# Kernel tuning notes

Hardware: AMD Instinct MI355X
Metric: run time of the kernel (lower is better)

Reference implementation:

```python
import math
import jax, jax.numpy as jnp
import numpy as np

# config (matches env defaults of the torch module, scaled to production size)
V, D, L, NH, NKV, MLP_M, RECUR, N_VB = 32768, 1024, 6, 16, 8, 3, 2, 5
BG_BK, BG_DIM = 4096, 128
HD = D // NH            # 64 head dim
KV = NKV * HD           # 512 kv width
B, T = 2, 1024
SOFTCAP = 30.0
EPS = 1.1920929e-07     # fp32 eps used by F.rms_norm(eps=None)


def _rms(x):
    return x * jax.lax.rsqrt(jnp.mean(jnp.square(x), axis=-1, keepdims=True) + EPS)


def _rope(x, c, s):
    h = x.shape[-1] // 2
    x1, x2 = x[..., :h], x[..., h:]
    return jnp.concatenate([x1 * c + x2 * s, -x1 * s + x2 * c], axis=-1)


def _forward(ids, tgt, emb, bg_embed, bg_proj, bg_scale, ve,
             Wq, Wk, Wv, Wo, qg, a_s, m_s, mix, Wfc, Wpr):
    Bz, Tz = ids.shape
    # token embedding + bigram-hash embedding
    x = emb[ids]
    t = ids.astype(jnp.int32)
    hv = jnp.bitwise_xor(t[:, 1:] * 36313, t[:, :-1] * 27191) % (BG_BK - 1)
    h = jnp.zeros_like(t).at[:, 1:].set(hv)
    bg = (bg_embed[h] @ bg_proj) * bg_scale
    x = _rms(x + bg)
    x0 = x
    # rope tables
    inv = 1.0 / (10000.0 ** (jnp.arange(0, HD, 2, dtype=jnp.float32) / HD))
    ang = jnp.arange(Tz, dtype=jnp.float32)[:, None] * inv      # (T, HD/2)
    c, s = jnp.cos(ang)[None, None], jnp.sin(ang)[None, None]   # (1,1,T,HD/2)
    mask = jnp.tril(jnp.ones((Tz, Tz), dtype=bool))
    eff = 0
    for _ in range(RECUR):
        for l in range(L):
            vel = ve[eff % N_VB][ids]                            # (B,T,KV)
            m = mix[l]
            x = m[0] * x + m[1] * x0
            # attention
            xn = _rms(x)
            q = (xn @ Wq[l]).reshape(Bz, Tz, NH, HD).transpose(0, 2, 1, 3)
            k = (xn @ Wk[l]).reshape(Bz, Tz, NKV, HD).transpose(0, 2, 1, 3)
            v = ((xn @ Wv[l]) + vel).reshape(Bz, Tz, NKV, HD).transpose(0, 2, 1, 3)
            q, k = _rms(q), _rms(k)
            q, k = _rope(q, c, s), _rope(k, c, s)
            q = q * qg[l][None, :, None, None]
            rep = NH // NKV                                      # GQA expand
            kf = jnp.repeat(k, rep, axis=1)
            vf = jnp.repeat(v, rep, axis=1)
            sc = jnp.einsum('bhqd,bhkd->bhqk', q, kf) / math.sqrt(HD)
            sc = jnp.where(mask, sc, -jnp.inf)
            att = jax.nn.softmax(sc, axis=-1)
            y = jnp.einsum('bhqk,bhkd->bhqd', att, vf)
            y = y.transpose(0, 2, 1, 3).reshape(Bz, Tz, D) @ Wo[l]
            x = x + a_s[l] * y
            # mlp: relu(fc(x))^2 @ proj
            hmid = jnp.square(jax.nn.relu(_rms(x) @ Wfc[l]))
            x = x + m_s[l] * (hmid @ Wpr[l])
            eff += 1
    x = _rms(x)
    lo = x @ emb.T
    lo = SOFTCAP * jnp.tanh(lo / SOFTCAP)
    logp = jax.nn.log_softmax(lo, axis=-1)
    nll = -jnp.take_along_axis(logp, tgt[..., None], axis=-1)[..., 0]
    return jnp.mean(nll)


def setup_inputs() -> dict:
    key = jax.random.key(0)
    ks = jax.random.split(key, 14)
    def nrm(k, shape, std):
        return std * jax.random.normal(k, shape, dtype=jnp.float32)
    eff = L * RECUR
    return {
        'ids': jax.random.randint(ks[0], (B, T), 0, V),
        'tgt': jax.random.randint(ks[1], (B, T), 0, V),
        'emb': nrm(ks[2], (V, D), 0.005),
        'bg_embed': nrm(ks[3], (BG_BK, BG_DIM), 0.02),
        'bg_proj': nrm(ks[4], (BG_DIM, D), 1.0 / math.sqrt(BG_DIM)),
        'bg_scale': jnp.float32(0.05),
        've': nrm(ks[5], (N_VB, V, KV), 0.01),
        'Wq': nrm(ks[6], (L, D, D), 1.0 / math.sqrt(D)),
        'Wk': nrm(ks[7], (L, D, KV), 1.0 / math.sqrt(D)),
        'Wv': nrm(ks[8], (L, D, KV), 1.0 / math.sqrt(D)),
        'Wo': nrm(ks[9], (L, D, D), 1.0 / (math.sqrt(D) * math.sqrt(2 * eff))),
        'qg': jnp.full((L, NH), 1.5, jnp.float32),
        'a_s': jnp.ones((L, D), jnp.float32),
        'm_s': jnp.ones((L, D), jnp.float32),
        'mix': jnp.stack([jnp.ones((L, D)), jnp.zeros((L, D))], axis=1).astype(jnp.float32),
        'Wfc': nrm(ks[10], (L, D, MLP_M * D), 1.0 / math.sqrt(D)),
        'Wpr': nrm(ks[11], (L, MLP_M * D, D), 1.0 / (math.sqrt(MLP_M * D) * math.sqrt(2 * eff))),
    }


def reference(ids, tgt, emb, bg_embed, bg_proj, bg_scale, ve,
              Wq, Wk, Wv, Wo, qg, a_s, m_s, mix, Wfc, Wpr):
    return _forward(ids, tgt, emb, bg_embed, bg_proj, bg_scale, ve,
                    Wq, Wk, Wv, Wo, qg, a_s, m_s, mix, Wfc, Wpr)
```

## Files before the change

kernel.cpp:

```cpp
#include <hip/hip_runtime.h>
#include <hip/hip_bf16.h>
#include <math.h>

#define DEV __device__ __forceinline__

typedef unsigned short u16;
typedef short bf16x8 __attribute__((ext_vector_type(8)));
typedef float f32x4 __attribute__((ext_vector_type(4)));
typedef u16 u16x8 __attribute__((ext_vector_type(8)));
typedef u16 u16x4 __attribute__((ext_vector_type(4)));

#define T_SEQ 1024
#define NTOK 2048
#define DIM 1024
#define NHD 16
#define NKVH 8
#define HDIM 64
#define KVD 512
#define MLPD 3072
#define VOC 32768
#define EPSF 1.1920929e-07f
#define SCAP 30.0f
#define NCB 512
#define PSTRIDE ((size_t)NTOK * DIM)

#define MEMFENCE asm volatile("" ::: "memory")

DEV u16 f2b(float f) {
  __hip_bfloat16 h = __float2bfloat16(f);
  u16 r; __builtin_memcpy(&r, &h, 2); return r;
}
DEV float b2f(u16 u) {
  __hip_bfloat16 h; __builtin_memcpy(&h, &u, 2);
  return __bfloat162float(h);
}

DEV void gload16(const void* g, void* l) {
  __builtin_amdgcn_global_load_lds((const __attribute__((address_space(1))) void*)g,
                                   (__attribute__((address_space(3))) void*)l, 16, 0, 0);
}

DEV float blk_sum256(float v, float* sbuf) {
#pragma unroll
  for (int o = 32; o; o >>= 1) v += __shfl_xor(v, o, 64);
  int w = threadIdx.x >> 6;
  if ((threadIdx.x & 63) == 0) sbuf[w] = v;
  __syncthreads();
  return sbuf[0] + sbuf[1] + sbuf[2] + sbuf[3];
}

__global__ __launch_bounds__(256) void prep_all(
    const float* __restrict__ Wq, const float* __restrict__ Wk, const float* __restrict__ Wv,
    const float* __restrict__ Wo, const float* __restrict__ Wfc, const float* __restrict__ Wpr,
    const float* __restrict__ emb,
    u16* __restrict__ WqkvT, u16* __restrict__ WoT, u16* __restrict__ WfcT,
    u16* __restrict__ WprT, u16* __restrict__ embB,
    float* __restrict__ rc, float* __restrict__ rs) {
  int bid = blockIdx.x;
  if (bid < 55296) {
    const float* in; u16* out; int nx, K, N; size_t in_ls, out_ls; int base;
    if (bid < 6144)       { base = 0;     in = Wq;  out = WqkvT;           nx = 32; K = 1024; N = 1024; in_ls = 1048576; out_ls = 2097152; }
    else if (bid < 9216)  { base = 6144;  in = Wk;  out = WqkvT + 1048576; nx = 16; K = 1024; N = 512;  in_ls = 524288;  out_ls = 2097152; }
    else if (bid < 12288) { base = 9216;  in = Wv;  out = WqkvT + 1572864; nx = 16; K = 1024; N = 512;  in_ls = 524288;  out_ls = 2097152; }
    else if (bid < 18432) { base = 12288; in = Wo;  out = WoT;             nx = 32; K = 1024; N = 1024; in_ls = 1048576; out_ls = 1048576; }
    else if (bid < 36864) { base = 18432; in = Wfc; out = WfcT;            nx = 96; K = 1024; N = 3072; in_ls = 3145728; out_ls = 3145728; }
    else                  { base = 36864; in = Wpr; out = WprT;            nx = 32; K = 3072; N = 1024; in_ls = 3145728; out_ls = 3145728; }
    int local = bid - base;
    int kx = local % nx;
    int rest = local / nx;
    int ny = K >> 5;
    int ky = rest % ny;
    int l = rest / ny;
    __shared__ float tile[32][33];
    const float* src = in + (size_t)l * in_ls;
    u16* dst = out + (size_t)l * out_ls;
    int k0 = ky << 5, n0 = kx << 5;
    int tx = threadIdx.x & 31, ty = threadIdx.x >> 5;
#pragma unroll
    for (int i = 0; i < 32; i += 8)
      tile[ty + i][tx] = src[(size_t)(k0 + ty + i) * N + n0 + tx];
    __syncthreads();
#pragma unroll
    for (int i = 0; i < 32; i += 8)
      dst[(size_t)(n0 + ty + i) * K + k0 + tx] = f2b(tile[tx][ty + i]);
  } else if (bid < 71680) {
    size_t i = ((size_t)(bid - 55296) * 256 + threadIdx.x) * 8;
    float4 a = *(const float4*)(emb + i);
    float4 b = *(const float4*)(emb + i + 4);
    u16x8 o;
    o[0] = f2b(a.x); o[1] = f2b(a.y); o[2] = f2b(a.z); o[3] = f2b(a.w);
    o[4] = f2b(b.x); o[5] = f2b(b.y); o[6] = f2b(b.z); o[7] = f2b(b.w);
    *(u16x8*)(embB + i) = o;
  } else {
    int idx = (bid - 71680) * 256 + threadIdx.x;
    int t = idx >> 5, i2 = idx & 31;
    float inv = expf(-((float)(2 * i2) / (float)HDIM) * logf(10000.0f));
    float ang = (float)t * inv;
    rc[idx] = cosf(ang);
    rs[idx] = sinf(ang);
  }
}

__global__ __launch_bounds__(256) void embed_kernel(const int* __restrict__ ids,
    const float* __restrict__ emb, const float* __restrict__ bg_embed,
    const float* __restrict__ bg_proj, const float* __restrict__ bg_scale_p,
    float* __restrict__ x, float* __restrict__ x0) {
  __shared__ float be[128];
  __shared__ float sbuf[4];
  int tok = blockIdx.x, tid = threadIdx.x;
  int t = tok & (T_SEQ - 1);
  int id = ids[tok];
  int hsh = 0;
  if (t > 0) {
    int prev = ids[tok - 1];
    hsh = ((id * 36313) ^ (prev * 27191)) % 4095;
  }
  if (tid < 128) be[tid] = bg_embed[hsh * 128 + tid];
  __syncthreads();
  float scale = bg_scale_p[0];
  const float4* bp = (const float4*)bg_proj;
  float ax = 0.f, ay = 0.f, az = 0.f, aw = 0.f;
#pragma unroll 4
  for (int j = 0; j < 128; ++j) {
    float bj = be[j];
    float4 p = bp[j * 256 + tid];
    ax += bj * p.x; ay += bj * p.y; az += bj * p.z; aw += bj * p.w;
  }
  float4 e = *(const float4*)(emb + (size_t)id * DIM + tid * 4);
  float vx = e.x + ax * scale, vy = e.y + ay * scale;
  float vz = e.z + az * scale, vw = e.w + aw * scale;
  float ss = vx * vx + vy * vy + vz * vz + vw * vw;
  float tot = blk_sum256(ss, sbuf);
  float rn = rsqrtf(tot * (1.0f / DIM) + EPSF);
  float4 o; o.x = vx * rn; o.y = vy * rn; o.z = vz * rn; o.w = vw * rn;
  size_t base = (size_t)tok * DIM + tid * 4;
  *(float4*)(x + base) = o;
  *(float4*)(x0 + base) = o;
}

template <int NP, int MIX>
__global__ __launch_bounds__(256) void norm_k(float* __restrict__ x,
    const float* __restrict__ parts, const float* __restrict__ colscale,
    const float* __restrict__ mixl, const float* __restrict__ x0,
    u16* __restrict__ xn) {
  __shared__ float sbuf[4];
  int tok = blockIdx.x, tid = threadIdx.x;
  size_t base = (size_t)tok * DIM + tid * 4;
  float4 a = *(const float4*)(x + base);
  if (NP > 0) {
    float4 cs = *(const float4*)(colscale + tid * 4);
    float4 s = *(const float4*)(parts + base);
    {
      float4 p = *(const float4*)(parts + PSTRIDE + base);
      s.x += p.x; s.y += p.y; s.z += p.z; s.w += p.w;
    }
    if (NP == 3) {
      float4 p = *(const float4*)(parts + 2 * PSTRIDE + base);
      s.x += p.x; s.y += p.y; s.z += p.z; s.w += p.w;
    }
    a.x += cs.x * s.x; a.y += cs.y * s.y; a.z += cs.z * s.z; a.w += cs.w * s.w;
  }
  if (MIX) {
    float4 m0 = *(const float4*)(mixl + tid * 4);
    float4 m1 = *(const float4*)(mixl + DIM + tid * 4);
    float4 b = *(const float4*)(x0 + base);
    a.x = m0.x * a.x + m1.x * b.x;
    a.y = m0.y * a.y + m1.y * b.y;
    a.z = m0.z * a.z + m1.z * b.z;
    a.w = m0.w * a.w + m1.w * b.w;
  }
  float ss = a.x * a.x + a.y * a.y + a.z * a.z + a.w * a.w;
  float tot = blk_sum256(ss, sbuf);
  float rn = rsqrtf(tot * (1.0f / DIM) + EPSF);
  if (NP > 0 || MIX) *(float4*)(x + base) = a;
  u16x4 q;
  q[0] = f2b(a.x * rn); q[1] = f2b(a.y * rn); q[2] = f2b(a.z * rn); q[3] = f2b(a.w * rn);
  *(u16x4*)(xn + base) = q;
}

template <int EPI, int BN>
__global__ __launch_bounds__(256, (BN == 64 ? 3 : 2)) void gemm_bt(
    const u16* __restrict__ A, const u16* __restrict__ Bt,
    float* __restrict__ Cf, u16* __restrict__ Cb,
    int N, int K, int kpn) {
  constexpr int MF = (BN == 128) ? 4 : 2;
  constexpr int ASZ = 128 * 64;
  constexpr int BSZ = BN * 64;
  constexpr int NLD = 4 + BN / 32;
  __shared__ u16 As[2 * ASZ];
  __shared__ u16 Bs[2 * BSZ];
  int tid = threadIdx.x;
  int wid = tid >> 6, lane = tid & 63;
  int g = lane >> 4, c = lane & 15;
  int row0 = blockIdx.y << 7, col0 = blockIdx.x * BN;
  int kbase = blockIdx.z * kpn;
  int wr = (BN == 128) ? ((wid >> 1) << 6) : (wid << 5);
  int wc = (BN == 128) ? ((wid & 1) << 6) : 0;
  f32x4 acc[MF][4] = {};

  int sr = lane >> 3;
  int kb = lane & 7;
  const u16* srcA[4];
  int ldsA[4];
#pragma unroll
  for (int i = 0; i < 4; ++i) {
    int s = (wid << 2) + i;
    int r = (s << 3) + sr;
    srcA[i] = A + (size_t)(row0 + r) * K + kbase + ((kb ^ (r & 7)) << 3);
    ldsA[i] = s << 9;
  }
  const u16* srcB[BN / 32];
  int ldsB[BN / 32];
#pragma unroll
  for (int i = 0; i < BN / 32; ++i) {
    int s = wid * (BN / 32) + i;
    int r = (s << 3) + sr;
    srcB[i] = Bt + (size_t)(col0 + r) * K + kbase + ((kb ^ (r & 7)) << 3);
    ldsB[i] = s << 9;
  }

#pragma unroll
  for (int i = 0; i < 4; ++i) gload16(srcA[i], As + ldsA[i]);
#pragma unroll
  for (int i = 0; i < BN / 32; ++i) gload16(srcB[i], Bs + ldsB[i]);

  int nk = kpn >> 6;
  for (int t = 0; t < nk; ++t) {
    int cur = t & 1;
    if (t + 1 < nk) {
      int nxt = cur ^ 1;
      int ko = (t + 1) << 6;
#pragma unroll
      for (int i = 0; i < 4; ++i) gload16(srcA[i] + ko, As + nxt * ASZ + ldsA[i]);
#pragma unroll
      for (int i = 0; i < BN / 32; ++i) gload16(srcB[i] + ko, Bs + nxt * BSZ + ldsB[i]);
      if constexpr (NLD == 6) asm volatile("s_waitcnt vmcnt(6)" ::: "memory");
      else asm volatile("s_waitcnt vmcnt(8)" ::: "memory");
    } else {
      asm volatile("s_waitcnt vmcnt(0)" ::: "memory");
    }
    __builtin_amdgcn_s_barrier();
    MEMFENCE;
    const u16* ab = As + cur * ASZ;
    const u16* bb = Bs + cur * BSZ;
#pragma unroll
    for (int ks = 0; ks < 2; ++ks) {
      bf16x8 af[MF], bfr[4];
#pragma unroll
      for (int m = 0; m < MF; ++m) {
        int r = wr + m * 16 + c;
        int kbs = ((ks << 2) + g) ^ (r & 7);
        af[m] = *(const bf16x8*)(ab + r * 64 + (kbs << 3));
      }
#pragma unroll
      for (int n = 0; n < 4; ++n) {
        int r = wc + n * 16 + c;
        int kbs = ((ks << 2) + g) ^ (r & 7);
        bfr[n] = *(const bf16x8*)(bb + r * 64 + (kbs << 3));
      }
      __builtin_amdgcn_s_setprio(1);
#pragma unroll
      for (int m = 0; m < MF; ++m)
#pragma unroll
        for (int n = 0; n < 4; ++n)
          acc[m][n] = __builtin_amdgcn_mfma_f32_16x16x32_bf16(af[m], bfr[n], acc[m][n], 0, 0, 0);
      __builtin_amdgcn_s_setprio(0);
    }
    MEMFENCE;
    __builtin_amdgcn_s_barrier();
  }

  size_t zoff = (size_t)blockIdx.z * PSTRIDE;
#pragma unroll
  for (int m = 0; m < MF; ++m) {
#pragma unroll
    for (int n = 0; n < 4; ++n) {
      int gcol = col0 + wc + n * 16 + c;
#pragma unroll
      for (int j = 0; j < 4; ++j) {
        int grow = row0 + wr + m * 16 + g * 4 + j;
        float v = acc[m][n][j];
        if (EPI == 1) {
          Cf[zoff + (size_t)grow * N + gcol] = v;
        } else if (EPI == 2) {
          float r = v > 0.f ? v : 0.f;
          Cb[(size_t)grow * N + gcol] = f2b(r * r);
        }
      }
    }
  }
}

__global__ __launch_bounds__(512, 2) void gemm_lmhead(
    const u16* __restrict__ A, const u16* __restrict__ Bt,
    const int* __restrict__ tgt, float* __restrict__ pM, float* __restrict__ pS,
    float* __restrict__ loTgt) {
  constexpr int K = 1024;
  constexpr int TSZ = 256 * 64;
  __shared__ u16 As[2 * TSZ];
  __shared__ u16 Bs[2 * TSZ];
  int tid = threadIdx.x;
  int wid = tid >> 6, lane = tid & 63;
  int wm = wid >> 2, wn = wid & 3;
  int g = lane >> 4, c = lane & 15;
  int bid = blockIdx.x;
  int swz = ((bid & 7) << 7) + (bid >> 3);
  int colb = swz >> 3, rowb = swz & 7;
  int row0 = rowb << 8, col0 = colb << 8;
  f32x4 acc[8][4] = {};

  int sr = lane >> 3, kb = lane & 7;
  const u16* srcA[4];
  const u16* srcB[4];
  int ldsOff[4];
#pragma unroll
  for (int i = 0; i < 4; ++i) {
    int s = (wid << 2) + i;
    int r = (s << 3) + sr;
    srcA[i] = A + (size_t)(row0 + r) * K + ((kb ^ (r & 7)) << 3);
    srcB[i] = Bt + (size_t)(col0 + r) * K + ((kb ^ (r & 7)) << 3);
    ldsOff[i] = s << 9;
  }

#pragma unroll
  for (int i = 0; i < 4; ++i) {
    gload16(srcA[i], As + ldsOff[i]);
    gload16(srcB[i], Bs + ldsOff[i]);
  }

  constexpr int nk = K >> 6;
  for (int kt = 0; kt < nk; ++kt) {
    int cur = kt & 1;
    if (kt + 1 < nk) {
      int nxt = cur ^ 1;
      int ko = (kt + 1) << 6;
#pragma unroll
      for (int i = 0; i < 4; ++i) {
        gload16(srcA[i] + ko, As + nxt * TSZ + ldsOff[i]);
        gload16(srcB[i] + ko, Bs + nxt * TSZ + ldsOff[i]);
      }
      asm volatile("s_waitcnt vmcnt(8)" ::: "memory");
    } else {
      asm volatile("s_waitcnt vmcnt(0)" ::: "memory");
    }
    __builtin_amdgcn_s_barrier();
    MEMFENCE;
    const u16* ab = As + cur * TSZ;
    const u16* bb = Bs + cur * TSZ;
    bf16x8 bfr[4][2];
#pragma unroll
    for (int nf = 0; nf < 4; ++nf) {
      int r = (wn << 6) + nf * 16 + c;
#pragma unroll
      for (int ks = 0; ks < 2; ++ks) {
        int kbs = ((ks << 2) + g) ^ (r & 7);
        bfr[nf][ks] = *(const bf16x8*)(bb + r * 64 + (kbs << 3));
      }
    }
#pragma unroll
    for (int p = 0; p < 4; ++p) {
      bf16x8 af[2][2];
#pragma unroll
      for (int mi = 0; mi < 2; ++mi) {
        int r = (wm << 7) + ((p << 1) + mi) * 16 + c;
#pragma unroll
        for (int ks = 0; ks < 2; ++ks) {
          int kbs = ((ks << 2) + g) ^ (r & 7);
          af[mi][ks] = *(const bf16x8*)(ab + r * 64 + (kbs << 3));
        }
      }
      __builtin_amdgcn_s_setprio(1);
#pragma unroll
      for (int ks = 0; ks < 2; ++ks)
#pragma unroll
        for (int mi = 0; mi < 2; ++mi)
#pragma unroll
          for (int nf = 0; nf < 4; ++nf)
            acc[(p << 1) + mi][nf] = __builtin_amdgcn_mfma_f32_16x16x32_bf16(
                af[mi][ks], bfr[nf][ks], acc[(p << 1) + mi][nf], 0, 0, 0);
      __builtin_amdgcn_s_setprio(0);
    }
    MEMFENCE;
    __builtin_amdgcn_s_barrier();
  }

  int cb = (col0 >> 6) + wn;
#pragma unroll
  for (int mf = 0; mf < 8; ++mf) {
#pragma unroll
    for (int j = 0; j < 4; ++j) {
      int grow = row0 + (wm << 7) + mf * 16 + g * 4 + j;
      int tg = tgt[grow];
      float sv[4];
      float mx = -3.0e38f;
#pragma unroll
      for (int nf = 0; nf < 4; ++nf) {
        float a = acc[mf][nf][j] * (1.0f / SCAP);
        a = fminf(fmaxf(a, -15.f), 15.f);
        float e = __expf(2.0f * a);
        float tt = SCAP * (e - 1.0f) / (e + 1.0f);
        sv[nf] = tt;
        mx = fmaxf(mx, tt);
        int gcol = col0 + (wn << 6) + nf * 16 + c;
        if (gcol == tg) loTgt[grow] = tt;
      }
      mx = fmaxf(mx, __shfl_xor(mx, 1, 64));
      mx = fmaxf(mx, __shfl_xor(mx, 2, 64));
      mx = fmaxf(mx, __shfl_xor(mx, 4, 64));
      mx = fmaxf(mx, __shfl_xor(mx, 8, 64));
      float s = 0.f;
#pragma unroll
      for (int nf = 0; nf < 4; ++nf) s += __expf(sv[nf] - mx);
      s += __shfl_xor(s, 1, 64);
      s += __shfl_xor(s, 2, 64);
      s += __shfl_xor(s, 4, 64);
      s += __shfl_xor(s, 8, 64);
      if (c == 0) {
        pM[(size_t)grow * NCB + cb] = mx;
        pS[(size_t)grow * NCB + cb] = s;
      }
    }
  }
}

__global__ __launch_bounds__(256, 3) void gemm_qkv(
    const u16* __restrict__ A, const u16* __restrict__ Bt,
    const float* __restrict__ qg_l, const float* __restrict__ rc, const float* __restrict__ rs,
    const float* __restrict__ ve, const int* __restrict__ ids, int vb,
    u16* __restrict__ qB, u16* __restrict__ kB, u16* __restrict__ vT) {
  constexpr int K = 1024;
  constexpr int ASZ = 128 * 64;
  constexpr int BSZ = 64 * 64;
  __shared__ u16 As[2 * ASZ];
  __shared__ u16 Bs[2 * BSZ];
  int tid = threadIdx.x;
  int wid = tid >> 6, lane = tid & 63;
  int g = lane >> 4, c = lane & 15;
  int bx = blockIdx.x;
  int row0 = blockIdx.y << 7, col0 = bx << 6;
  f32x4 acc[2][4] = {};

  int sr = lane >> 3, kb = lane & 7;
  const u16* srcA[4];
  int ldsA[4];
#pragma unroll
  for (int i = 0; i < 4; ++i) {
    int s = (wid << 2) + i;
    int r = (s << 3) + sr;
    srcA[i] = A + (size_t)(row0 + r) * K + ((kb ^ (r & 7)) << 3);
    ldsA[i] = s << 9;
  }
  const u16* srcB[2];
  int ldsB[2];
#pragma unroll
  for (int i = 0; i < 2; ++i) {
    int s = (wid << 1) + i;
    int r = (s << 3) + sr;
    srcB[i] = Bt + (size_t)(col0 + r) * K + ((kb ^ (r & 7)) << 3);
    ldsB[i] = s << 9;
  }

#pragma unroll
  for (int i = 0; i < 4; ++i) gload16(srcA[i], As + ldsA[i]);
#pragma unroll
  for (int i = 0; i < 2; ++i) gload16(srcB[i], Bs + ldsB[i]);

  for (int t = 0; t < 16; ++t) {
    int cur = t & 1;
    if (t + 1 < 16) {
      int nxt = cur ^ 1;
      int ko = (t + 1) << 6;
#pragma unroll
      for (int i = 0; i < 4; ++i) gload16(srcA[i] + ko, As + nxt * ASZ + ldsA[i]);
#pragma unroll
      for (int i = 0; i < 2; ++i) gload16(srcB[i] + ko, Bs + nxt * BSZ + ldsB[i]);
      asm volatile("s_waitcnt vmcnt(6)" ::: "memory");
    } else {
      asm volatile("s_waitcnt vmcnt(0)" ::: "memory");
    }
    __builtin_amdgcn_s_barrier();
    MEMFENCE;
    const u16* ab = As + cur * ASZ;
    const u16* bb = Bs + cur * BSZ;
#pragma unroll
    for (int ks = 0; ks < 2; ++ks) {
      bf16x8 af[2], bfr[4];
#pragma unroll
      for (int m = 0; m < 2; ++m) {
        int r = (wid << 5) + m * 16 + c;
        int kbs = ((ks << 2) + g) ^ (r & 7);
        af[m] = *(const bf16x8*)(ab + r * 64 + (kbs << 3));
      }
#pragma unroll
      for (int n = 0; n < 4; ++n) {
        int r = n * 16 + c;
        int kbs = ((ks << 2) + g) ^ (r & 7);
        bfr[n] = *(const bf16x8*)(bb + r * 64 + (kbs << 3));
      }
      __builtin_amdgcn_s_setprio(1);
#pragma unroll
      for (int m = 0; m < 2; ++m)
#pragma unroll
        for (int n = 0; n < 4; ++n)
          acc[m][n] = __builtin_amdgcn_mfma_f32_16x16x32_bf16(af[m], bfr[n], acc[m][n], 0, 0, 0);
      __builtin_amdgcn_s_setprio(0);
    }
    MEMFENCE;
    __builtin_amdgcn_s_barrier();
  }

  int b = row0 >> 10;
  if (bx < 24) {
    bool isq = (bx < 16);
    int h = isq ? bx : bx - 16;
    float gmul = isq ? qg_l[h] * 0.125f : 1.0f;
    u16* hb = isq ? (qB + ((size_t)(b * NHD + h)) * T_SEQ * HDIM)
                  : (kB + ((size_t)(b * NKVH + h)) * T_SEQ * HDIM);
#pragma unroll
    for (int m = 0; m < 2; ++m) {
#pragma unroll
      for (int j = 0; j < 4; ++j) {
        int grow = row0 + (wid << 5) + m * 16 + g * 4 + j;
        int t = grow & (T_SEQ - 1);
        float vv[4];
        float ss = 0.f;
#pragma unroll
        for (int n = 0; n < 4; ++n) { vv[n] = acc[m][n][j]; ss += vv[n] * vv[n]; }
        ss += __shfl_xor(ss, 1, 64);
        ss += __shfl_xor(ss, 2, 64);
        ss += __shfl_xor(ss, 4, 64);
        ss += __shfl_xor(ss, 8, 64);
        float rn = rsqrtf(ss * (1.0f / HDIM) + EPSF);
#pragma unroll
        for (int n = 0; n < 4; ++n) vv[n] *= rn;
        float c0 = rc[t * 32 + c], s0 = rs[t * 32 + c];
        float c1 = rc[t * 32 + 16 + c], s1 = rs[t * 32 + 16 + c];
        float o0 = vv[0] * c0 + vv[2] * s0;
        float o1 = vv[1] * c1 + vv[3] * s1;
        float o2 = vv[2] * c0 - vv[0] * s0;
        float o3 = vv[3] * c1 - vv[1] * s1;
        u16* dst = hb + (size_t)t * HDIM;
        dst[c] = f2b(o0 * gmul);
        dst[16 + c] = f2b(o1 * gmul);
        dst[32 + c] = f2b(o2 * gmul);
        dst[48 + c] = f2b(o3 * gmul);
      }
    }
  } else {
    int kh = bx - 24;
#pragma unroll
    for (int m = 0; m < 2; ++m) {
#pragma unroll
      for (int j = 0; j < 4; ++j) {
        int grow = row0 + (wid << 5) + m * 16 + g * 4 + j;
        int lr = (wid << 5) + m * 16 + g * 4 + j;
        int id = ids[grow];
        const float* vl = ve + ((size_t)vb * VOC + id) * KVD + kh * HDIM;
#pragma unroll
        for (int n = 0; n < 4; ++n)
          As[lr * 72 + n * 16 + c] = f2b(acc[m][n][j] + vl[n * 16 + c]);
      }
    }
    __syncthreads();
    int hd = tid & 63, seg = tid >> 6;
    int t0 = (row0 & (T_SEQ - 1)) + seg * 32;
    u16* dst = vT + (((size_t)(b * NKVH + kh)) * HDIM + hd) * T_SEQ + t0;
#pragma unroll
    for (int i = 0; i < 32; i += 8) {
      u16x8 o;
#pragma unroll
      for (int e = 0; e < 8; ++e) o[e] = As[(seg * 32 + i + e) * 72 + hd];
      *(u16x8*)(dst + i) = o;
    }
  }
}

__global__ __launch_bounds__(128) void attn_kernel(const u16* __restrict__ qB,
    const u16* __restrict__ kB, const u16* __restrict__ vT, const float* __restrict__ qg_l,
    float* __restrict__ oPart, float* __restrict__ lPart) {
  __shared__ u16 plds[2][32 * 76];
  int z = blockIdx.z;
  int b = z & 1, half = z >> 1;
  int h = blockIdx.y;
  int kh = h >> 1;
  int wid = threadIdx.x >> 6, lane = threadIdx.x & 63;
  int g = lane >> 4, c = lane & 15;
  int strip = wid ? (31 - (int)blockIdx.x) : (int)blockIdx.x;
  int qr0 = strip << 5;
  const u16* qptr = qB + ((size_t)(b * NHD + h)) * T_SEQ * HDIM;
  const u16* kptr = kB + ((size_t)(b * NKVH + kh)) * T_SEQ * HDIM;
  const u16* vptr = vT + ((size_t)(b * NKVH + kh)) * HDIM * T_SEQ;
  u16* pw = plds[wid];
  float Mh = fabsf(qg_l[h]) * 8.0f;

  bf16x8 aq[2][2];
#pragma unroll
  for (int m = 0; m < 2; ++m)
#pragma unroll
    for (int ks = 0; ks < 2; ++ks)
      aq[m][ks] = *(const bf16x8*)(qptr + (qr0 + m * 16 + c) * HDIM + ks * 32 + g * 8);

  bf16x8 vone;
#pragma unroll
  for (int e = 0; e < 8; ++e) vone[e] = (short)0x3F80;

  f32x4 oacc[2][4] = {};
  f32x4 lacc[2] = {};

  bf16x8 kR0[4][2], vR0[4][2], kR1[4][2], vR1[4][2];

  auto LOADKV = [&](bf16x8 (&bk)[4][2], bf16x8 (&bv)[4][2], int kv0) {
#pragma unroll
    for (int n = 0; n < 4; ++n)
#pragma unroll
      for (int ks = 0; ks < 2; ++ks) {
        bk[n][ks] = *(const bf16x8*)(kptr + (kv0 + n * 16 + c) * HDIM + ks * 32 + g * 8);
        bv[n][ks] = *(const bf16x8*)(vptr + (n * 16 + c) * T_SEQ + kv0 + ks * 32 + g * 8);
      }
  };

  auto BODY = [&](bf16x8 (&bk)[4][2], bf16x8 (&bv)[4][2], int kv0) {
    f32x4 sc[2][4] = {};
#pragma unroll
    for (int ks = 0; ks < 2; ++ks)
#pragma unroll
      for (int m = 0; m < 2; ++m)
#pragma unroll
        for (int n = 0; n < 4; ++n)
          sc[m][n] = __builtin_amdgcn_mfma_f32_16x16x32_bf16(aq[m][ks], bk[n][ks], sc[m][n], 0, 0, 0);
    bool maskT = (kv0 + 64 > qr0);
#pragma unroll
    for (int m = 0; m < 2; ++m) {
#pragma unroll
      for (int j = 0; j < 4; ++j) {
        int row = qr0 + m * 16 + g * 4 + j;
        float p0 = __expf(sc[m][0][j] - Mh);
        float p1 = __expf(sc[m][1][j] - Mh);
        float p2 = __expf(sc[m][2][j] - Mh);
        float p3 = __expf(sc[m][3][j] - Mh);
        if (maskT) {
          if (kv0 + c > row) p0 = 0.f;
          if (kv0 + 16 + c > row) p1 = 0.f;
          if (kv0 + 32 + c > row) p2 = 0.f;
          if (kv0 + 48 + c > row) p3 = 0.f;
        }
        int pr = m * 16 + g * 4 + j;
        pw[pr * 76 + c] = f2b(p0);
        pw[pr * 76 + 16 + c] = f2b(p1);
        pw[pr * 76 + 32 + c] = f2b(p2);
        pw[pr * 76 + 48 + c] = f2b(p3);
      }
    }
    MEMFENCE;
    bf16x8 ap[2][2];
#pragma unroll
    for (int m = 0; m < 2; ++m)
#pragma unroll
      for (int ks = 0; ks < 2; ++ks) {
        u16x8 tmp = *(const u16x8*)(pw + (m * 16 + c) * 76 + ks * 32 + g * 8);
        __builtin_memcpy(&ap[m][ks], &tmp, 16);
      }
#pragma unroll
    for (int ks = 0; ks < 2; ++ks) {
#pragma unroll
      for (int m = 0; m < 2; ++m) {
#pragma unroll
        for (int n = 0; n < 4; ++n)
          oacc[m][n] = __builtin_amdgcn_mfma_f32_16x16x32_bf16(ap[m][ks], bv[n][ks], oacc[m][n], 0, 0, 0);
        lacc[m] = __builtin_amdgcn_mfma_f32_16x16x32_bf16(ap[m][ks], vone, lacc[m], 0, 0, 0);
      }
    }
  };

  int kv0 = half << 6;
  if (kv0 <= qr0) {
    LOADKV(kR0, vR0, kv0);
    while (true) {
      int nxt = kv0 + 128;
      if (nxt <= qr0) LOADKV(kR1, vR1, nxt);
      BODY(kR0, vR0, kv0);
      kv0 = nxt;
      if (kv0 > qr0) break;
      nxt = kv0 + 128;
      if (nxt <= qr0) LOADKV(kR0, vR0, nxt);
      BODY(kR1, vR1, kv0);
      kv0 = nxt;
      if (kv0 > qr0) break;
    }
  }

  size_t pbase = (size_t)((half * 2 + b) * NHD + h) * T_SEQ;
#pragma unroll
  for (int m = 0; m < 2; ++m) {
#pragma unroll
    for (int j = 0; j < 4; ++j) {
      int trow = qr0 + m * 16 + g * 4 + j;
      float* orow = oPart + (pbase + trow) * HDIM;
#pragma unroll
      for (int n = 0; n < 4; ++n)
        orow[n * 16 + c] = oacc[m][n][j];
      if (c == 0) lPart[pbase + trow] = lacc[m][j];
    }
  }
}

__global__ __launch_bounds__(256) void attn_merge(const float* __restrict__ oPart,
    const float* __restrict__ lPart, u16* __restrict__ attout) {
  int tok = blockIdx.x;
  int b = tok >> 10, t = tok & (T_SEQ - 1);
  int col = threadIdx.x << 2;
  int h = col >> 6, d = col & 63;
  size_t i0 = (size_t)((0 * 2 + b) * NHD + h) * T_SEQ + t;
  size_t i1 = (size_t)((1 * 2 + b) * NHD + h) * T_SEQ + t;
  float4 o0 = *(const float4*)(oPart + i0 * HDIM + d);
  float4 o1 = *(const float4*)(oPart + i1 * HDIM + d);
  float inv = 1.0f / (lPart[i0] + lPart[i1]);
  u16x4 q;
  q[0] = f2b((o0.x + o1.x) * inv);
  q[1] = f2b((o0.y + o1.y) * inv);
  q[2] = f2b((o0.z + o1.z) * inv);
  q[3] = f2b((o0.w + o1.w) * inv);
  *(u16x4*)(attout + (size_t)tok * DIM + col) = q;
}

__global__ __launch_bounds__(256) void lse_merge(const float* __restrict__ pM,
    const float* __restrict__ pS, const float* __restrict__ loTgt, float* __restrict__ nll) {
  __shared__ float sbuf[4];
  int tok = blockIdx.x, tid = threadIdx.x;
  int wid = tid >> 6, lane = tid & 63;
  const float* rm = pM + (size_t)tok * NCB;
  const float* rs = pS + (size_t)tok * NCB;
  float m0 = rm[tid], m1 = rm[tid + 256];
  float mx = fmaxf(m0, m1);
#pragma unroll
  for (int o = 32; o; o >>= 1) mx = fmaxf(mx, __shfl_xor(mx, o, 64));
  if (lane == 0) sbuf[wid] = mx;
  __syncthreads();
  float M = fmaxf(fmaxf(sbuf[0], sbuf[1]), fmaxf(sbuf[2], sbuf[3]));
  __syncthreads();
  float s = rs[tid] * __expf(m0 - M) + rs[tid + 256] * __expf(m1 - M);
  float S = blk_sum256(s, sbuf);
  if (tid == 0) nll[tok] = logf(S) + M - loTgt[tok];
}

__global__ __launch_bounds__(256) void loss_final(const float* __restrict__ nll,
    float* __restrict__ out) {
  __shared__ float sbuf[4];
  int tid = threadIdx.x;
  float acc = 0.f;
  for (int i = tid; i < NTOK; i += 256) acc += nll[i];
  float tot = blk_sum256(acc, sbuf);
  if (tid == 0) out[0] = tot * (1.0f / NTOK);
}

extern "C" void kernel_launch(void* const* d_in, const int* in_sizes, int n_in,
                              void* d_out, int out_size, void* d_ws, size_t ws_size,
                              hipStream_t stream) {
  (void)in_sizes; (void)n_in; (void)out_size; (void)ws_size;
  const int* ids = (const int*)d_in[0];
  const int* tgt = (const int*)d_in[1];
  const float* emb = (const float*)d_in[2];
  const float* bg_embed = (const float*)d_in[3];
  const float* bg_proj = (const float*)d_in[4];
  const float* bg_scale = (const float*)d_in[5];
  const float* ve = (const float*)d_in[6];
  const float* Wq = (const float*)d_in[7];
  const float* Wk = (const float*)d_in[8];
  const float* Wv = (const float*)d_in[9];
  const float* Wo = (const float*)d_in[10];
  const float* qg = (const float*)d_in[11];
  const float* a_s = (const float*)d_in[12];
  const float* m_s = (const float*)d_in[13];
  const float* mix = (const float*)d_in[14];
  const float* Wfc = (const float*)d_in[15];
  const float* Wpr = (const float*)d_in[16];

  char* w = (char*)d_ws;
  auto alloc = [&](size_t bytes) {
    char* p = w;
    w += (bytes + 255) & ~(size_t)255;
    return p;
  };
  u16* WqkvT = (u16*)alloc(6ull * 2048 * 1024 * 2);
  u16* WoT   = (u16*)alloc(6ull * 1024 * 1024 * 2);
  u16* WfcT  = (u16*)alloc(6ull * 3072 * 1024 * 2);
  u16* WprT  = (u16*)alloc(6ull * 1024 * 3072 * 2);
  u16* embB  = (u16*)alloc((size_t)VOC * DIM * 2);
  float* x   = (float*)alloc((size_t)NTOK * DIM * 4);
  float* x0  = (float*)alloc((size_t)NTOK * DIM * 4);
  u16* xn    = (u16*)alloc((size_t)NTOK * DIM * 2);
  u16* qBuf  = (u16*)alloc((size_t)NTOK * DIM * 2);
  u16* kBuf  = (u16*)alloc((size_t)NTOK * KVD * 2);
  u16* vTb   = (u16*)alloc((size_t)NTOK * KVD * 2);
  u16* attout = (u16*)alloc((size_t)NTOK * DIM * 2);
  u16* xmlp  = (u16*)alloc((size_t)NTOK * DIM * 2);
  u16* hmid  = (u16*)alloc((size_t)NTOK * MLPD * 2);
  float* pparts = (float*)alloc(3 * PSTRIDE * 4);
  float* rc  = (float*)alloc((size_t)T_SEQ * 32 * 4);
  float* rs  = (float*)alloc((size_t)T_SEQ * 32 * 4);
  float* pM  = (float*)alloc((size_t)NTOK * NCB * 4);
  float* pS  = (float*)alloc((size_t)NTOK * NCB * 4);
  float* loTgt = (float*)alloc(NTOK * 4);
  float* nll = (float*)alloc(NTOK * 4);
  float* oPart = (float*)alloc(4ull * NHD * T_SEQ * HDIM * 4);
  float* lPart = (float*)alloc(4ull * NHD * T_SEQ * 4);

  prep_all<<<71808, 256, 0, stream>>>(Wq, Wk, Wv, Wo, Wfc, Wpr, emb,
      WqkvT, WoT, WfcT, WprT, embB, rc, rs);
  embed_kernel<<<NTOK, 256, 0, stream>>>(ids, emb, bg_embed, bg_proj, bg_scale, x, x0);

  int lprev = 0;
  for (int step = 0; step < 12; ++step) {
    int l = step % 6;
    if (step == 0)
      norm_k<0, 1><<<NTOK, 256, 0, stream>>>(x, nullptr, nullptr, mix + l * 2048, x0, xn);
    else
      norm_k<3, 1><<<NTOK, 256, 0, stream>>>(x, pparts, m_s + lprev * DIM, mix + l * 2048, x0, xn);
    gemm_qkv<<<dim3(32, 16), 256, 0, stream>>>(xn, WqkvT + (size_t)l * 2048 * 1024,
        qg + l * 16, rc, rs, ve, ids, step % 5, qBuf, kBuf, vTb);
    attn_kernel<<<dim3(16, 16, 4), 128, 0, stream>>>(qBuf, kBuf, vTb, qg + l * 16,
        oPart, lPart);
    attn_merge<<<NTOK, 256, 0, stream>>>(oPart, lPart, attout);
    gemm_bt<1, 64><<<dim3(16, 16, 2), 256, 0, stream>>>(attout, WoT + (size_t)l * 1024 * 1024,
        pparts, nullptr, 1024, 1024, 512);
    norm_k<2, 0><<<NTOK, 256, 0, stream>>>(x, pparts, a_s + l * DIM, nullptr, nullptr, xmlp);
    gemm_bt<2, 64><<<dim3(48, 16, 1), 256, 0, stream>>>(xmlp, WfcT + (size_t)l * 3072 * 1024,
        nullptr, hmid, 3072, 1024, 1024);
    gemm_bt<1, 64><<<dim3(16, 16, 3), 256, 0, stream>>>(hmid, WprT + (size_t)l * 1024 * 3072,
        pparts, nullptr, 1024, 3072, 1024);
    lprev = l;
  }

  norm_k<3, 0><<<NTOK, 256, 0, stream>>>(x, pparts, m_s + lprev * DIM, nullptr, nullptr, xn);
  gemm_lmhead<<<1024, 512, 0, stream>>>(xn, embB, tgt, pM, pS, loTgt);
  lse_merge<<<NTOK, 256, 0, stream>>>(pM, pS, loTgt, nll);
  loss_final<<<1, 256, 0, stream>>>(nll, (float*)d_out);
}
```

Before: 1.942 ms.

## Drop attention KV split and merge kernel; fuse first norm into embed

Attention now handles the full causal KV range per block, with no two-way KV split, and normalizes and writes bf16 output directly. This removes the attn_merge kernel and its fp32 partial buffers. Separately, the first layer's mix and RMSNorm are folded into the embedding kernel, removing one norm launch. The trade-off is half as many attention blocks, so each block runs a longer serial KV loop and the GPU may be less full.

```diff
diff --git a/kernel.cpp b/kernel.cpp
--- a/kernel.cpp
+++ b/kernel.cpp
@@ -104,7 +104,8 @@
 __global__ __launch_bounds__(256) void embed_kernel(const int* __restrict__ ids,
     const float* __restrict__ emb, const float* __restrict__ bg_embed,
     const float* __restrict__ bg_proj, const float* __restrict__ bg_scale_p,
-    float* __restrict__ x, float* __restrict__ x0) {
+    const float* __restrict__ mix0,
+    float* __restrict__ x, float* __restrict__ x0, u16* __restrict__ xn) {
   __shared__ float be[128];
   __shared__ float sbuf[4];
   int tok = blockIdx.x, tid = threadIdx.x;
@@ -134,8 +135,22 @@
   float rn = rsqrtf(tot * (1.0f / DIM) + EPSF);
   float4 o; o.x = vx * rn; o.y = vy * rn; o.z = vz * rn; o.w = vw * rn;
   size_t base = (size_t)tok * DIM + tid * 4;
-  *(float4*)(x + base) = o;
   *(float4*)(x0 + base) = o;
+  float4 m0 = *(const float4*)(mix0 + tid * 4);
+  float4 m1 = *(const float4*)(mix0 + DIM + tid * 4);
+  float4 a;
+  a.x = (m0.x + m1.x) * o.x;
+  a.y = (m0.y + m1.y) * o.y;
+  a.z = (m0.z + m1.z) * o.z;
+  a.w = (m0.w + m1.w) * o.w;
+  *(float4*)(x + base) = a;
+  __syncthreads();
+  float ss2 = a.x * a.x + a.y * a.y + a.z * a.z + a.w * a.w;
+  float tot2 = blk_sum256(ss2, sbuf);
+  float rn2 = rsqrtf(tot2 * (1.0f / DIM) + EPSF);
+  u16x4 q;
+  q[0] = f2b(a.x * rn2); q[1] = f2b(a.y * rn2); q[2] = f2b(a.z * rn2); q[3] = f2b(a.w * rn2);
+  *(u16x4*)(xn + base) = q;
 }
 
 template <int NP, int MIX>
@@ -577,11 +592,9 @@
 
 __global__ __launch_bounds__(128) void attn_kernel(const u16* __restrict__ qB,
     const u16* __restrict__ kB, const u16* __restrict__ vT, const float* __restrict__ qg_l,
-    float* __restrict__ oPart, float* __restrict__ lPart) {
+    u16* __restrict__ attout) {
   __shared__ u16 plds[2][32 * 76];
-  int z = blockIdx.z;
-  int b = z & 1, half = z >> 1;
-  int h = blockIdx.y;
+  int b = blockIdx.z, h = blockIdx.y;
   int kh = h >> 1;
   int wid = threadIdx.x >> 6, lane = threadIdx.x & 63;
   int g = lane >> 4, c = lane & 15;
@@ -672,55 +685,31 @@
     }
   };
 
-  int kv0 = half << 6;
-  if (kv0 <= qr0) {
-    LOADKV(kR0, vR0, kv0);
-    while (true) {
-      int nxt = kv0 + 128;
-      if (nxt <= qr0) LOADKV(kR1, vR1, nxt);
-      BODY(kR0, vR0, kv0);
-      kv0 = nxt;
-      if (kv0 > qr0) break;
-      nxt = kv0 + 128;
-      if (nxt <= qr0) LOADKV(kR0, vR0, nxt);
-      BODY(kR1, vR1, kv0);
-      kv0 = nxt;
-      if (kv0 > qr0) break;
-    }
-  }
-
-  size_t pbase = (size_t)((half * 2 + b) * NHD + h) * T_SEQ;
+  LOADKV(kR0, vR0, 0);
+  int kv0 = 0;
+  while (true) {
+    if (kv0 + 64 <= qr0) LOADKV(kR1, vR1, kv0 + 64);
+    BODY(kR0, vR0, kv0);
+    kv0 += 64;
+    if (kv0 > qr0) break;
+    if (kv0 + 64 <= qr0) LOADKV(kR0, vR0, kv0 + 64);
+    BODY(kR1, vR1, kv0);
+    kv0 += 64;
+    if (kv0 > qr0) break;
+  }
+
 #pragma unroll
   for (int m = 0; m < 2; ++m) {
 #pragma unroll
     for (int j = 0; j < 4; ++j) {
+      float inv = 1.0f / lacc[m][j];
       int trow = qr0 + m * 16 + g * 4 + j;
-      float* orow = oPart + (pbase + trow) * HDIM;
+      u16* orow = attout + ((size_t)(b * T_SEQ + trow)) * DIM + h * HDIM;
 #pragma unroll
       for (int n = 0; n < 4; ++n)
-        orow[n * 16 + c] = oacc[m][n][j];
-      if (c == 0) lPart[pbase + trow] = lacc[m][j];
-    }
-  }
-}
-
-__global__ __launch_bounds__(256) void attn_merge(const float* __restrict__ oPart,
-    const float* __restrict__ lPart, u16* __restrict__ attout) {
-  int tok = blockIdx.x;
-  int b = tok >> 10, t = tok & (T_SEQ - 1);
-  int col = threadIdx.x << 2;
-  int h = col >> 6, d = col & 63;
-  size_t i0 = (size_t)((0 * 2 + b) * NHD + h) * T_SEQ + t;
-  size_t i1 = (size_t)((1 * 2 + b) * NHD + h) * T_SEQ + t;
-  float4 o0 = *(const float4*)(oPart + i0 * HDIM + d);
-  float4 o1 = *(const float4*)(oPart + i1 * HDIM + d);
-  float inv = 1.0f / (lPart[i0] + lPart[i1]);
-  u16x4 q;
-  q[0] = f2b((o0.x + o1.x) * inv);
-  q[1] = f2b((o0.y + o1.y) * inv);
-  q[2] = f2b((o0.z + o1.z) * inv);
-  q[3] = f2b((o0.w + o1.w) * inv);
-  *(u16x4*)(attout + (size_t)tok * DIM + col) = q;
+        orow[n * 16 + c] = f2b(oacc[m][n][j] * inv);
+    }
+  }
 }
 
 __global__ __launch_bounds__(256) void lse_merge(const float* __restrict__ pM,
@@ -802,25 +791,20 @@
   float* pS  = (float*)alloc((size_t)NTOK * NCB * 4);
   float* loTgt = (float*)alloc(NTOK * 4);
   float* nll = (float*)alloc(NTOK * 4);
-  float* oPart = (float*)alloc(4ull * NHD * T_SEQ * HDIM * 4);
-  float* lPart = (float*)alloc(4ull * NHD * T_SEQ * 4);
 
   prep_all<<<71808, 256, 0, stream>>>(Wq, Wk, Wv, Wo, Wfc, Wpr, emb,
       WqkvT, WoT, WfcT, WprT, embB, rc, rs);
-  embed_kernel<<<NTOK, 256, 0, stream>>>(ids, emb, bg_embed, bg_proj, bg_scale, x, x0);
+  embed_kernel<<<NTOK, 256, 0, stream>>>(ids, emb, bg_embed, bg_proj, bg_scale,
+      mix, x, x0, xn);
 
   int lprev = 0;
   for (int step = 0; step < 12; ++step) {
     int l = step % 6;
-    if (step == 0)
-      norm_k<0, 1><<<NTOK, 256, 0, stream>>>(x, nullptr, nullptr, mix + l * 2048, x0, xn);
-    else
+    if (step > 0)
       norm_k<3, 1><<<NTOK, 256, 0, stream>>>(x, pparts, m_s + lprev * DIM, mix + l * 2048, x0, xn);
     gemm_qkv<<<dim3(32, 16), 256, 0, stream>>>(xn, WqkvT + (size_t)l * 2048 * 1024,
         qg + l * 16, rc, rs, ve, ids, step % 5, qBuf, kBuf, vTb);
-    attn_kernel<<<dim3(16, 16, 4), 128, 0, stream>>>(qBuf, kBuf, vTb, qg + l * 16,
-        oPart, lPart);
-    attn_merge<<<NTOK, 256, 0, stream>>>(oPart, lPart, attout);
+    attn_kernel<<<dim3(16, 16, 2), 128, 0, stream>>>(qBuf, kBuf, vTb, qg + l * 16, attout);
     gemm_bt<1, 64><<<dim3(16, 16, 2), 256, 0, stream>>>(attout, WoT + (size_t)l * 1024 * 1024,
         pparts, nullptr, 1024, 1024, 512);
     norm_k<2, 0><<<NTOK, 256, 0, stream>>>(x, pparts, a_s + l * DIM, nullptr, nullptr, xmlp);
```

New measurement: 1.844 ms. 1.05x faster.
